# Performance work log

Measured on AMD Instinct MI355X. Metric: run time of the kernel, lower is better.

Reference implementation:

```python
import jax, jax.numpy as jnp
import numpy as np

E, HEADS, HD, L, FF = 768, 12, 64, 12, 3072


def layernorm(x, g, b, eps=1e-5):
    m = jnp.mean(x, axis=-1, keepdims=True)
    v = jnp.var(x, axis=-1, keepdims=True)
    return (x - m) / jnp.sqrt(v + eps) * g + b


def setup_inputs() -> dict:
    key = jax.random.key(0)
    ks = jax.random.split(key, 26)
    B, N, PS = 32, 1024, 24
    P2 = PS * PS
    def rn(k, shape, s=0.02):
        return jax.random.normal(k, shape, dtype=jnp.float32) * s
    return {
        "scene_masks": jax.random.normal(ks[0], (B, N, PS, PS), dtype=jnp.float32),
        "target_mask": jax.random.normal(ks[1], (B, PS, PS), dtype=jnp.float32),
        "emb_W": rn(ks[2], (E, P2)),            # torch Linear weight [out,in]
        "emb_b": rn(ks[3], (E,)),
        "class_embed": rn(ks[4], (1, 1, E)),
        "scene_pos": rn(ks[5], (1, N + 1, E)),
        "target_pos": rn(ks[6], (1, 2, E)),
        "ln1_g": jnp.ones((L, E), jnp.float32),
        "ln1_b": jnp.zeros((L, E), jnp.float32),
        "ln2_g": jnp.ones((L, E), jnp.float32),
        "ln2_b": jnp.zeros((L, E), jnp.float32),
        "Wq": rn(ks[7], (L, HD, HD)),
        "Wk": rn(ks[8], (L, HD, HD)),
        "Wv": rn(ks[9], (L, HD, HD)),
        "Wo": rn(ks[10], (L, E, E)),
        "bo": rn(ks[11], (L, E)),
        "W1": rn(ks[12], (L, FF, E)),
        "b1": rn(ks[13], (L, FF)),
        "W2": rn(ks[14], (L, E, FF)),
        "b2": rn(ks[15], (L, E)),
        "mlp_W": rn(ks[16], (N, E)),
        "mlp_b": rn(ks[17], (N,)),
    }


def _forward_logits(scene_masks, target_mask, emb_W, emb_b, class_embed, scene_pos,
                    target_pos, ln1_g, ln1_b, ln2_g, ln2_b, Wq, Wk, Wv, Wo, bo,
                    W1, b1, W2, b2, mlp_W, mlp_b):
    B, N, H, W = scene_masks.shape
    P2 = H * W
    scene = scene_masks.reshape(B, N, P2) @ emb_W.T + emb_b          # [B,N,E]
    tgt = target_mask.reshape(B, 1, P2) @ emb_W.T + emb_b            # [B,1,E]
    cls = jnp.broadcast_to(class_embed, (B, 1, E))
    scene = jnp.concatenate([cls, scene], axis=1) + scene_pos[:, :N + 1]  # [B,N+1,E]
    tgt = jnp.concatenate([cls, tgt], axis=1) + target_pos               # [B,2,E]
    scale = jnp.sqrt(jnp.float32(E))

    def block(tq, p):
        g1, bb1n, g2, bb2n, wq, wk, wv, wo, bo_, w1, b1_, w2, b2_ = p
        kv = layernorm(scene, g1, bb1n)                # norm1(value)=norm1(key)
        q = layernorm(tq, g1, bb1n)                    # norm1(query)
        kvh = kv.reshape(B, N + 1, HEADS, HD)
        qh = q.reshape(B, 2, HEADS, HD)
        # per-head Linear shares one [HD,HD] weight across all heads
        qs = jnp.einsum('nqhd,ed->nqhe', qh, wq)
        ks_ = jnp.einsum('nkhd,ed->nkhe', kvh, wk)
        vs = jnp.einsum('nkhd,ed->nkhe', kvh, wv)
        energy = jnp.einsum('nqhd,nkhd->nhqk', qs, ks_)     # [B,H,2,N+1]
        att = jax.nn.softmax(energy / scale, axis=-1)
        out = jnp.einsum('nhqk,nkhd->nqhd', att, vs).reshape(B, 2, E)
        out = out @ wo.T + bo_
        x = layernorm(out + tq, g1, bb1n)
        ff = jax.nn.relu(x @ w1.T + b1_) @ w2.T + b2_
        return layernorm(ff + x, g2, bb2n), None

    params = (ln1_g, ln1_b, ln2_g, ln2_b, Wq, Wk, Wv, Wo, bo, W1, b1, W2, b2)
    tgt, _ = jax.lax.scan(block, tgt, params)
    x = jnp.mean(tgt, axis=1) @ mlp_W.T + mlp_b       # [B, num_patches]
    return x


def reference(scene_masks, target_mask, emb_W, emb_b, class_embed, scene_pos,
              target_pos, ln1_g, ln1_b, ln2_g, ln2_b, Wq, Wk, Wv, Wo, bo,
              W1, b1, W2, b2, mlp_W, mlp_b):
    x = _forward_logits(scene_masks, target_mask, emb_W, emb_b, class_embed,
                        scene_pos, target_pos, ln1_g, ln1_b, ln2_g, ln2_b,
                        Wq, Wk, Wv, Wo, bo, W1, b1, W2, b2, mlp_W, mlp_b)
    # sorted_nodes = argsort desc + 1; eye(P+1)[nodes-1] == one_hot(argsort desc)
    order = jnp.argsort(-x, axis=1)[:, :5]                # top-5 patch indices
    return jax.nn.one_hot(order, x.shape[1] + 1, dtype=jnp.float32)  # [B,5,P+1]
```

## Files before the change

### kernel.cpp

```cpp
#include <hip/hip_runtime.h>
#include <math.h>

#define E_DIM 768
#define NTOK 1025
#define B_DIM 32
#define NHEADS 12
#define HDIM 64
#define LAYERS 12
#define FF_DIM 3072
#define P2 576

__device__ __forceinline__ float block_reduce_sum(float v, float* red) {
  int tid = threadIdx.x;
  red[tid] = v;
  __syncthreads();
#pragma unroll
  for (int s = 128; s > 0; s >>= 1) {
    if (tid < s) red[tid] += red[tid + s];
    __syncthreads();
  }
  float r = red[0];
  __syncthreads();
  return r;
}

__global__ __launch_bounds__(256) void embed_gemm(
    const float* __restrict__ A, const float* __restrict__ W,
    const float* __restrict__ bias, const float* __restrict__ pos,
    float* __restrict__ scene) {
  __shared__ float Xs[16][132];
  __shared__ float Ws[16][132];
  int tid = threadIdx.x;
  int bid = blockIdx.x;
  int xcd = bid & 7;
  int idx = bid >> 3;
  int m_tile = xcd * 32 + idx / 6;
  int n_tile = idx % 6;
  int n0 = n_tile * 128;
  int m0 = m_tile * 128;
  int lr = tid >> 2;
  int lk = (tid & 3) << 2;
  int ty = tid >> 4, tx = tid & 15;
  float acc[8][8] = {};
  for (int k0 = 0; k0 < P2; k0 += 16) {
    float4 x0 = *(const float4*)(A + (size_t)(m0 + lr) * P2 + k0 + lk);
    float4 x1 = *(const float4*)(A + (size_t)(m0 + 64 + lr) * P2 + k0 + lk);
    float4 w0 = *(const float4*)(W + (size_t)(n0 + lr) * P2 + k0 + lk);
    float4 w1 = *(const float4*)(W + (size_t)(n0 + 64 + lr) * P2 + k0 + lk);
    __syncthreads();
    Xs[lk + 0][lr] = x0.x; Xs[lk + 1][lr] = x0.y; Xs[lk + 2][lr] = x0.z; Xs[lk + 3][lr] = x0.w;
    Xs[lk + 0][64 + lr] = x1.x; Xs[lk + 1][64 + lr] = x1.y; Xs[lk + 2][64 + lr] = x1.z; Xs[lk + 3][64 + lr] = x1.w;
    Ws[lk + 0][lr] = w0.x; Ws[lk + 1][lr] = w0.y; Ws[lk + 2][lr] = w0.z; Ws[lk + 3][lr] = w0.w;
    Ws[lk + 0][64 + lr] = w1.x; Ws[lk + 1][64 + lr] = w1.y; Ws[lk + 2][64 + lr] = w1.z; Ws[lk + 3][64 + lr] = w1.w;
    __syncthreads();
#pragma unroll
    for (int kk = 0; kk < 16; ++kk) {
      float4 a0 = *(const float4*)&Xs[kk][ty << 2];
      float4 a1 = *(const float4*)&Xs[kk][64 + (ty << 2)];
      float4 b0 = *(const float4*)&Ws[kk][tx << 2];
      float4 b1 = *(const float4*)&Ws[kk][64 + (tx << 2)];
      float av[8] = {a0.x, a0.y, a0.z, a0.w, a1.x, a1.y, a1.z, a1.w};
      float bv[8] = {b0.x, b0.y, b0.z, b0.w, b1.x, b1.y, b1.z, b1.w};
#pragma unroll
      for (int i = 0; i < 8; ++i)
#pragma unroll
        for (int j = 0; j < 8; ++j) acc[i][j] += av[i] * bv[j];
    }
  }
#pragma unroll
  for (int i = 0; i < 8; ++i) {
    int mloc = (i < 4) ? ((ty << 2) + i) : (64 + (ty << 2) + i - 4);
    int m = m0 + mloc;
    int b = m >> 10, nt = m & 1023;
    size_t row = ((size_t)b * NTOK + 1 + nt) * E_DIM;
    size_t prow = (size_t)(1 + nt) * E_DIM;
#pragma unroll
    for (int half = 0; half < 2; ++half) {
      int n = n0 + half * 64 + (tx << 2);
      float4 o4;
      o4.x = acc[i][half * 4 + 0] + bias[n + 0] + pos[prow + n + 0];
      o4.y = acc[i][half * 4 + 1] + bias[n + 1] + pos[prow + n + 1];
      o4.z = acc[i][half * 4 + 2] + bias[n + 2] + pos[prow + n + 2];
      o4.w = acc[i][half * 4 + 3] + bias[n + 3] + pos[prow + n + 3];
      *(float4*)&scene[row + n] = o4;
    }
  }
}

__global__ void scene_cls(const float* __restrict__ cls, const float* __restrict__ pos,
                          float* __restrict__ scene) {
  int b = blockIdx.x;
  for (int e = threadIdx.x; e < E_DIM; e += 256)
    scene[(size_t)b * NTOK * E_DIM + e] = cls[e] + pos[e];
}

__global__ __launch_bounds__(256) void ln_rows(const float* __restrict__ in, float* __restrict__ out) {
  __shared__ float red[256];
  int r = blockIdx.x, tid = threadIdx.x;
  const float* x = in + (size_t)r * E_DIM;
  float a0 = x[tid], a1 = x[tid + 256], a2 = x[tid + 512];
  float mean = block_reduce_sum(a0 + a1 + a2, red) * (1.f / 768.f);
  float d0 = a0 - mean, d1 = a1 - mean, d2 = a2 - mean;
  float var = block_reduce_sum(d0 * d0 + d1 * d1 + d2 * d2, red) * (1.f / 768.f);
  float rinv = rsqrtf(var + 1e-5f);
  float* o = out + (size_t)r * E_DIM;
  o[tid] = d0 * rinv; o[tid + 256] = d1 * rinv; o[tid + 512] = d2 * rinv;
}

__global__ __launch_bounds__(256) void tgt_init(
    const float* __restrict__ tmask, const float* __restrict__ W,
    const float* __restrict__ bias, const float* __restrict__ cls,
    const float* __restrict__ tpos, float* __restrict__ tq) {
  int b = blockIdx.x, tid = threadIdx.x;
  for (int e = tid; e < E_DIM; e += 256)
    tq[(size_t)(b * 2) * E_DIM + e] = cls[e] + tpos[e];
  const float* tm = tmask + (size_t)b * P2;
  for (int e = tid; e < E_DIM; e += 256) {
    const float* wr = W + (size_t)e * P2;
    float s = 0.f;
    for (int k = 0; k < P2; k += 4) {
      float4 w4 = *(const float4*)&wr[k];
      float4 t4 = *(const float4*)&tm[k];
      s += w4.x * t4.x + w4.y * t4.y + w4.z * t4.z + w4.w * t4.w;
    }
    tq[(size_t)(b * 2 + 1) * E_DIM + e] = s + bias[e] + tpos[E_DIM + e];
  }
}

__global__ void prep_m(const float* __restrict__ Wq, const float* __restrict__ Wk,
                       float* __restrict__ Mb) {
  int l = blockIdx.y;
  int idx = blockIdx.x * 256 + threadIdx.x;
  int d = idx >> 6, dp = idx & 63;
  const float* wq = Wq + l * 4096;
  const float* wk = Wk + l * 4096;
  float s = 0.f;
#pragma unroll 8
  for (int e = 0; e < 64; ++e) s += wq[e * 64 + d] * wk[e * 64 + dp];
  Mb[l * 4096 + idx] = s;
}

__global__ void prep_wvo(const float* __restrict__ Wv, const float* __restrict__ Wo,
                         float* __restrict__ Wvo) {
  int l = blockIdx.y;
  int idx = blockIdx.x * 256 + threadIdx.x;
  int ep = idx / 768, hd = idx % 768;
  int h = hd >> 6, d = hd & 63;
  const float* wv = Wv + (size_t)l * 4096;
  const float* wo = Wo + (size_t)l * 768 * 768 + (size_t)ep * 768 + h * 64;
  float s = 0.f;
#pragma unroll 8
  for (int ev = 0; ev < 64; ++ev) s += wv[ev * 64 + d] * wo[ev];
  Wvo[(size_t)l * 589824 + idx] = s;
}

#define ACH 272
__global__ __launch_bounds__(256) void attn_flash_q(
    const float* __restrict__ tq_in, const float* __restrict__ partFF,
    const float* __restrict__ fb2l, const float* __restrict__ g2l,
    const float* __restrict__ b2l, const float* __restrict__ xres,
    int from_part, float* __restrict__ tq_out,
    const float* __restrict__ Mb, const float* __restrict__ g1,
    const float* __restrict__ b1, int l,
    const float* __restrict__ ns, float* __restrict__ ctx) {
  __shared__ float red[256];
  __shared__ float qs[2][64];
  __shared__ float qg[2][64];
  __shared__ float qmb[2];
  __shared__ float sred[2][16];
  __shared__ float cred[2][16][64];
  int b = blockIdx.x / NHEADS;
  int h = blockIdx.x % NHEADS;
  int tid = threadIdx.x;
  const float* gl = g1 + l * E_DIM;
  const float* bl = b1 + l * E_DIM;
  int seg = h >> 2;
  int base = h * 64 - seg * 256;

  float y[2][3];
  if (!from_part) {
#pragma unroll
    for (int r = 0; r < 2; ++r) {
      const float* x = tq_in + (size_t)(b * 2 + r) * E_DIM;
      y[r][0] = x[tid]; y[r][1] = x[tid + 256]; y[r][2] = x[tid + 512];
    }
  } else {
#pragma unroll
    for (int r = 0; r < 2; ++r) {
      int m = b * 2 + r;
      float t[3];
#pragma unroll
      for (int c = 0; c < 3; ++c) {
        int n = tid + c * 256;
        float s = 0.f;
        for (int i = 0; i < 16; ++i) s += partFF[((size_t)i * 64 + m) * 768 + n];
        t[c] = s + fb2l[n] + xres[(size_t)m * 768 + n];
      }
      float mean = block_reduce_sum(t[0] + t[1] + t[2], red) * (1.f / 768.f);
      float d0 = t[0] - mean, d1 = t[1] - mean, d2 = t[2] - mean;
      float var = block_reduce_sum(d0 * d0 + d1 * d1 + d2 * d2, red) * (1.f / 768.f);
      float rinv = rsqrtf(var + 1e-5f);
      y[r][0] = d0 * rinv * g2l[tid] + b2l[tid];
      y[r][1] = d1 * rinv * g2l[tid + 256] + b2l[tid + 256];
      y[r][2] = d2 * rinv * g2l[tid + 512] + b2l[tid + 512];
      if (h == 0) {
        tq_out[(size_t)m * E_DIM + tid] = y[r][0];
        tq_out[(size_t)m * E_DIM + tid + 256] = y[r][1];
        tq_out[(size_t)m * E_DIM + tid + 512] = y[r][2];
      }
    }
  }

  for (int r = 0; r < 2; ++r) {
    float a0 = y[r][0], a1 = y[r][1], a2 = y[r][2];
    float mean = block_reduce_sum(a0 + a1 + a2, red) * (1.f / 768.f);
    float d0 = a0 - mean, d1 = a1 - mean, d2 = a2 - mean;
    float var = block_reduce_sum(d0 * d0 + d1 * d1 + d2 * d2, red) * (1.f / 768.f);
    float rinv = rsqrtf(var + 1e-5f);
    float dv = (seg == 0) ? d0 : ((seg == 1) ? d1 : d2);
    if (tid >= base && tid < base + 64) {
      int d = tid - base;
      qs[r][d] = dv * rinv * gl[h * 64 + d] + bl[h * 64 + d];
    }
  }
  __syncthreads();
  const float inv_scale = rsqrtf(768.f);
  if (tid < 128) {
    int r = tid >> 6, dp = tid & 63;
    const float* M = Mb + l * 4096;
    float s = 0.f;
#pragma unroll 8
    for (int d = 0; d < 64; ++d) s += qs[r][d] * M[d * 64 + dp];
    qg[r][dp] = s * gl[h * 64 + dp] * inv_scale;
    red[tid] = s * bl[h * 64 + dp];
  }
  __syncthreads();
  if (tid < 2) {
    float a = 0.f;
    for (int dp = 0; dp < 64; ++dp) a += red[tid * 64 + dp];
    qmb[tid] = a * inv_scale;
  }
  __syncthreads();
  int g = tid >> 4;
  int lane = tid & 15;
  int r0 = b * 2, r1 = r0 + 1;
  const float* nsb = ns + (size_t)b * NTOK * E_DIM + h * 64;
  float4 q0v = *(const float4*)&qg[0][lane * 4];
  float4 q1v = *(const float4*)&qg[1][lane * 4];
  float qb0 = qmb[0], qb1 = qmb[1];
  float m = -1e30f, s0 = 0.f, s1 = 0.f;
  float4 c0 = {0, 0, 0, 0}, c1 = {0, 0, 0, 0};
  float4 v[17];
  float e0a[17], e1a[17];
  for (int cb = 0; cb < NTOK; cb += ACH) {
    int ntk = NTOK - cb; if (ntk > ACH) ntk = ACH;
    int cnt = (ntk - g + 15) >> 4;
    float mloc = -1e30f;
#pragma unroll
    for (int i = 0; i < 17; ++i) {
      if (i < cnt) {
        int k = cb + g + (i << 4);
        float4 vv = *(const float4*)(nsb + (size_t)k * E_DIM + lane * 4);
        v[i] = vv;
        float p0 = vv.x * q0v.x + vv.y * q0v.y + vv.z * q0v.z + vv.w * q0v.w;
        float p1 = vv.x * q1v.x + vv.y * q1v.y + vv.z * q1v.z + vv.w * q1v.w;
#pragma unroll
        for (int off = 8; off; off >>= 1) {
          p0 += __shfl_xor(p0, off, 16);
          p1 += __shfl_xor(p1, off, 16);
        }
        float e0 = p0 + qb0, e1 = p1 + qb1;
        e0a[i] = e0; e1a[i] = e1;
        mloc = fmaxf(mloc, fmaxf(e0, e1));
      }
    }
    red[tid] = mloc;
    __syncthreads();
#pragma unroll
    for (int s = 128; s > 0; s >>= 1) {
      if (tid < s) red[tid] = fmaxf(red[tid], red[tid + s]);
      __syncthreads();
    }
    float mnew = fmaxf(m, red[0]);
    __syncthreads();
    if (mnew > m) {
      float f = expf(m - mnew);
      s0 *= f; s1 *= f;
      c0.x *= f; c0.y *= f; c0.z *= f; c0.w *= f;
      c1.x *= f; c1.y *= f; c1.z *= f; c1.w *= f;
      m = mnew;
    }
#pragma unroll
    for (int i = 0; i < 17; ++i) {
      if (i < cnt) {
        float p0 = expf(e0a[i] - m);
        float p1 = expf(e1a[i] - m);
        s0 += p0; s1 += p1;
        c0.x += p0 * v[i].x; c0.y += p0 * v[i].y; c0.z += p0 * v[i].z; c0.w += p0 * v[i].w;
        c1.x += p1 * v[i].x; c1.y += p1 * v[i].y; c1.z += p1 * v[i].z; c1.w += p1 * v[i].w;
      }
    }
  }
  if (lane == 0) { sred[0][g] = s0; sred[1][g] = s1; }
  *(float4*)&cred[0][g][lane * 4] = c0;
  *(float4*)&cred[1][g][lane * 4] = c1;
  __syncthreads();
  if (tid < 128) {
    int t = tid >> 6, dd = tid & 63;
    int o = h * 64 + dd;
    float stot = 0.f, cs = 0.f;
#pragma unroll
    for (int gg = 0; gg < 16; ++gg) { stot += sred[t][gg]; cs += cred[t][gg][dd]; }
    float inv = 1.f / stot;
    ctx[(size_t)(r0 + t) * E_DIM + o] = cs * inv * gl[o] + bl[o];
  }
}

__global__ __launch_bounds__(256) void skinny_part(
    const float* __restrict__ X, int K, const float* __restrict__ W,
    int kchunk, float* __restrict__ part, int N) {
  __shared__ float Xs[16][64];
  __shared__ float Ws[16][64];
  int tid = threadIdx.x;
  int n0 = blockIdx.x * 64;
  int s = blockIdx.y;
  int kbeg = s * kchunk;
  int lr = tid >> 2;
  int lk = (tid & 3) << 2;
  int ty = tid >> 4, tx = tid & 15;
  float acc[4][4] = {};
  for (int k0 = kbeg; k0 < kbeg + kchunk; k0 += 16) {
    float4 xv = *(const float4*)(X + (size_t)lr * K + k0 + lk);
    float4 wv = *(const float4*)(W + (size_t)(n0 + lr) * K + k0 + lk);
    __syncthreads();
    Xs[lk + 0][lr] = xv.x; Xs[lk + 1][lr] = xv.y; Xs[lk + 2][lr] = xv.z; Xs[lk + 3][lr] = xv.w;
    Ws[lk + 0][lr] = wv.x; Ws[lk + 1][lr] = wv.y; Ws[lk + 2][lr] = wv.z; Ws[lk + 3][lr] = wv.w;
    __syncthreads();
#pragma unroll
    for (int kk = 0; kk < 16; ++kk) {
      float4 a4 = *(const float4*)&Xs[kk][ty << 2];
      float4 b4 = *(const float4*)&Ws[kk][tx << 2];
      float av[4] = {a4.x, a4.y, a4.z, a4.w};
      float bv[4] = {b4.x, b4.y, b4.z, b4.w};
#pragma unroll
      for (int i = 0; i < 4; ++i)
#pragma unroll
        for (int j = 0; j < 4; ++j) acc[i][j] += av[i] * bv[j];
    }
  }
#pragma unroll
  for (int i = 0; i < 4; ++i) {
    int mm = (ty << 2) + i;
    float4 o4 = make_float4(acc[i][0], acc[i][1], acc[i][2], acc[i][3]);
    *(float4*)&part[((size_t)s * 64 + mm) * N + n0 + (tx << 2)] = o4;
  }
}

__global__ __launch_bounds__(256) void skinny_h1_part(
    const float* __restrict__ part1, const float* __restrict__ b1,
    const float* __restrict__ W, int kchunk, float* __restrict__ part2) {
  __shared__ float Xs[16][64];
  __shared__ float Ws[16][64];
  const int K = 3072, N = 768;
  int tid = threadIdx.x;
  int n0 = blockIdx.x * 64;
  int s = blockIdx.y;
  int kbeg = s * kchunk;
  int lr = tid >> 2;
  int lk = (tid & 3) << 2;
  int ty = tid >> 4, tx = tid & 15;
  float acc[4][4] = {};
  for (int k0 = kbeg; k0 < kbeg + kchunk; k0 += 16) {
    float4 x0 = *(const float4*)(part1 + (size_t)lr * K + k0 + lk);
    float4 x1 = *(const float4*)(part1 + (size_t)(64 + lr) * K + k0 + lk);
    float4 x2 = *(const float4*)(part1 + (size_t)(128 + lr) * K + k0 + lk);
    float4 x3 = *(const float4*)(part1 + (size_t)(192 + lr) * K + k0 + lk);
    float4 bb = *(const float4*)(b1 + k0 + lk);
    float4 xv;
    xv.x = fmaxf(x0.x + x1.x + x2.x + x3.x + bb.x, 0.f);
    xv.y = fmaxf(x0.y + x1.y + x2.y + x3.y + bb.y, 0.f);
    xv.z = fmaxf(x0.z + x1.z + x2.z + x3.z + bb.z, 0.f);
    xv.w = fmaxf(x0.w + x1.w + x2.w + x3.w + bb.w, 0.f);
    float4 wv = *(const float4*)(W + (size_t)(n0 + lr) * K + k0 + lk);
    __syncthreads();
    Xs[lk + 0][lr] = xv.x; Xs[lk + 1][lr] = xv.y; Xs[lk + 2][lr] = xv.z; Xs[lk + 3][lr] = xv.w;
    Ws[lk + 0][lr] = wv.x; Ws[lk + 1][lr] = wv.y; Ws[lk + 2][lr] = wv.z; Ws[lk + 3][lr] = wv.w;
    __syncthreads();
#pragma unroll
    for (int kk = 0; kk < 16; ++kk) {
      float4 a4 = *(const float4*)&Xs[kk][ty << 2];
      float4 b4 = *(const float4*)&Ws[kk][tx << 2];
      float av[4] = {a4.x, a4.y, a4.z, a4.w};
      float bv[4] = {b4.x, b4.y, b4.z, b4.w};
#pragma unroll
      for (int i = 0; i < 4; ++i)
#pragma unroll
        for (int j = 0; j < 4; ++j) acc[i][j] += av[i] * bv[j];
    }
  }
#pragma unroll
  for (int i = 0; i < 4; ++i) {
    int mm = (ty << 2) + i;
    float4 o4 = make_float4(acc[i][0], acc[i][1], acc[i][2], acc[i][3]);
    *(float4*)&part2[((size_t)s * 64 + mm) * N + n0 + (tx << 2)] = o4;
  }
}

__global__ __launch_bounds__(256) void reduce_ln(
    const float* __restrict__ part, int S, const float* __restrict__ bias,
    const float* __restrict__ res, const float* __restrict__ g,
    const float* __restrict__ bsh, float* __restrict__ out,
    float* __restrict__ xmean) {
  __shared__ float red[256];
  int m = blockIdx.x, tid = threadIdx.x;
  float t[3];
#pragma unroll
  for (int c = 0; c < 3; ++c) {
    int n = tid + c * 256;
    float s = 0.f;
    for (int i = 0; i < S; ++i) s += part[((size_t)i * 64 + m) * 768 + n];
    t[c] = s + bias[n] + res[(size_t)m * 768 + n];
  }
  float mean = block_reduce_sum(t[0] + t[1] + t[2], red) * (1.f / 768.f);
  float d0 = t[0] - mean, d1 = t[1] - mean, d2 = t[2] - mean;
  float var = block_reduce_sum(d0 * d0 + d1 * d1 + d2 * d2, red) * (1.f / 768.f);
  float rinv = rsqrtf(var + 1e-5f);
  float y0 = d0 * rinv * g[tid] + bsh[tid];
  float y1 = d1 * rinv * g[tid + 256] + bsh[tid + 256];
  float y2 = d2 * rinv * g[tid + 512] + bsh[tid + 512];
  out[(size_t)m * 768 + tid] = y0;
  out[(size_t)m * 768 + tid + 256] = y1;
  out[(size_t)m * 768 + tid + 512] = y2;
  if (xmean) {
    float* xr = xmean + (size_t)(m >> 1) * 768;
    atomicAdd(&xr[tid], 0.5f * y0);
    atomicAdd(&xr[tid + 256], 0.5f * y1);
    atomicAdd(&xr[tid + 512], 0.5f * y2);
  }
}

__global__ __launch_bounds__(256) void top5_from_parts(
    const float* __restrict__ part, const float* __restrict__ bias,
    float* __restrict__ out) {
  __shared__ float v[1024];
  __shared__ float bv[256];
  __shared__ int bi[256];
  int b = blockIdx.x, tid = threadIdx.x;
  for (int i = tid; i < 1024; i += 256) {
    float s = part[(size_t)(0 * 64 + b) * 1024 + i] + part[(size_t)(1 * 64 + b) * 1024 + i] +
              part[(size_t)(2 * 64 + b) * 1024 + i] + part[(size_t)(3 * 64 + b) * 1024 + i];
    v[i] = s + bias[i];
  }
  float* ob = out + (size_t)b * 5 * NTOK;
  for (int i = tid; i < 5 * NTOK; i += 256) ob[i] = 0.f;
  __syncthreads();
  for (int it = 0; it < 5; ++it) {
    float best = -1e38f;
    int bidx = 0x7fffffff;
    for (int i = tid; i < 1024; i += 256) {
      float x = v[i];
      if (x > best || (x == best && i < bidx)) { best = x; bidx = i; }
    }
    bv[tid] = best; bi[tid] = bidx;
    __syncthreads();
    for (int s = 128; s > 0; s >>= 1) {
      if (tid < s) {
        if (bv[tid + s] > bv[tid] || (bv[tid + s] == bv[tid] && bi[tid + s] < bi[tid])) {
          bv[tid] = bv[tid + s]; bi[tid] = bi[tid + s];
        }
      }
      __syncthreads();
    }
    if (tid == 0) {
      ob[it * NTOK + bi[0]] = 1.0f;
      v[bi[0]] = -1e38f;
    }
    __syncthreads();
  }
}

extern "C" void kernel_launch(void* const* d_in, const int* in_sizes, int n_in,
                              void* d_out, int out_size, void* d_ws, size_t ws_size,
                              hipStream_t stream) {
  const float* scene_masks = (const float*)d_in[0];
  const float* target_mask = (const float*)d_in[1];
  const float* emb_W = (const float*)d_in[2];
  const float* emb_b = (const float*)d_in[3];
  const float* class_embed = (const float*)d_in[4];
  const float* scene_pos = (const float*)d_in[5];
  const float* target_pos = (const float*)d_in[6];
  const float* ln1_g = (const float*)d_in[7];
  const float* ln1_b = (const float*)d_in[8];
  const float* ln2_g = (const float*)d_in[9];
  const float* ln2_b = (const float*)d_in[10];
  const float* Wq = (const float*)d_in[11];
  const float* Wk = (const float*)d_in[12];
  const float* Wv = (const float*)d_in[13];
  const float* Wo = (const float*)d_in[14];
  const float* bo = (const float*)d_in[15];
  const float* W1 = (const float*)d_in[16];
  const float* fb1 = (const float*)d_in[17];
  const float* W2 = (const float*)d_in[18];
  const float* fb2 = (const float*)d_in[19];
  const float* mlp_W = (const float*)d_in[20];
  const float* mlp_b = (const float*)d_in[21];
  float* out = (float*)d_out;

  float* ws = (float*)d_ws;
  float* scene = ws;
  float* Mbuf = scene + 25190400;
  float* Wvo = Mbuf + 49152;
  float* tq = Wvo + 7077888;
  float* ctxf = tq + 49152;
  float* xbuf = ctxf + 49152;
  float* xm = xbuf + 49152;
  float* partA = xm + 49152;
  float* partB = partA + 786432;

  embed_gemm<<<1536, 256, 0, stream>>>(scene_masks, emb_W, emb_b, scene_pos, scene);
  scene_cls<<<32, 256, 0, stream>>>(class_embed, scene_pos, scene);
  ln_rows<<<32 * NTOK, 256, 0, stream>>>(scene, scene);
  tgt_init<<<32, 256, 0, stream>>>(target_mask, emb_W, emb_b, class_embed, target_pos, tq);
  prep_m<<<dim3(16, 12), 256, 0, stream>>>(Wq, Wk, Mbuf);
  prep_wvo<<<dim3(2304, 12), 256, 0, stream>>>(Wv, Wo, Wvo);
  hipMemsetAsync(xm, 0, 49152 * sizeof(float), stream);

  for (int l = 0; l < LAYERS; ++l) {
    if (l == 0)
      attn_flash_q<<<32 * NHEADS, 256, 0, stream>>>(
          tq, nullptr, nullptr, nullptr, nullptr, nullptr, 0, nullptr,
          Mbuf, ln1_g, ln1_b, l, scene, ctxf);
    else
      attn_flash_q<<<32 * NHEADS, 256, 0, stream>>>(
          nullptr, partA, fb2 + (l - 1) * 768, ln2_g + (l - 1) * 768,
          ln2_b + (l - 1) * 768, xbuf, 1, tq,
          Mbuf, ln1_g, ln1_b, l, scene, ctxf);
    skinny_part<<<dim3(12, 8), 256, 0, stream>>>(ctxf, 768, Wvo + (size_t)l * 589824, 96, partA, 768);
    reduce_ln<<<64, 256, 0, stream>>>(partA, 8, bo + l * 768, tq,
                                      ln1_g + l * 768, ln1_b + l * 768, xbuf, nullptr);
    skinny_part<<<dim3(48, 4), 256, 0, stream>>>(xbuf, 768, W1 + (size_t)l * FF_DIM * 768, 192, partB, FF_DIM);
    skinny_h1_part<<<dim3(12, 16), 256, 0, stream>>>(partB, fb1 + l * FF_DIM,
                                                     W2 + (size_t)l * 768 * FF_DIM, 192, partA);
  }
  reduce_ln<<<64, 256, 0, stream>>>(partA, 16, fb2 + 11 * 768, xbuf,
                                    ln2_g + 11 * 768, ln2_b + 11 * 768, tq, xm);

  skinny_part<<<dim3(16, 4), 256, 0, stream>>>(xm, 768, mlp_W, 192, partA, 1024);
  top5_from_parts<<<32, 256, 0, stream>>>(partA, mlp_b, out);
}
```

Baseline: 1.817 ms.

## Fuse per-head output projection into attention kernel, drop separate skinny GEMM

Each attention block now multiplies its per-head context by the matching column slice of the fused Wv·Wo matrix and writes per-head partial sums, which reduce_ln sums over 12 heads. This removes one GEMM launch and the context buffer round trip per layer. In exchange every block re-reads its 768x64 weight slice (shared across batches via cache) and partC adds a larger partial buffer to reduce.

```diff
diff --git a/kernel.cpp b/kernel.cpp
--- a/kernel.cpp
+++ b/kernel.cpp
@@ -162,13 +162,16 @@
     int from_part, float* __restrict__ tq_out,
     const float* __restrict__ Mb, const float* __restrict__ g1,
     const float* __restrict__ b1, int l,
-    const float* __restrict__ ns, float* __restrict__ ctx) {
+    const float* __restrict__ ns, const float* __restrict__ Wvo_l,
+    float* __restrict__ partC) {
   __shared__ float red[256];
   __shared__ float qs[2][64];
   __shared__ float qg[2][64];
   __shared__ float qmb[2];
   __shared__ float sred[2][16];
   __shared__ float cred[2][16][64];
+  __shared__ float ctxs[2][64];
+  __shared__ float pr[2][768];
   int b = blockIdx.x / NHEADS;
   int h = blockIdx.x % NHEADS;
   int tid = threadIdx.x;
@@ -312,7 +315,28 @@
 #pragma unroll
     for (int gg = 0; gg < 16; ++gg) { stot += sred[t][gg]; cs += cred[t][gg][dd]; }
     float inv = 1.f / stot;
-    ctx[(size_t)(r0 + t) * E_DIM + o] = cs * inv * gl[o] + bl[o];
+    ctxs[t][dd] = cs * inv * gl[o] + bl[o];
+  }
+  __syncthreads();
+  const float* wbase = Wvo_l + (size_t)h * 64 + lane * 4;
+  float4 x0 = *(const float4*)&ctxs[0][lane * 4];
+  float4 x1 = *(const float4*)&ctxs[1][lane * 4];
+  for (int n = g; n < 768; n += 16) {
+    float4 wv = *(const float4*)(wbase + (size_t)n * 768);
+    float a0 = wv.x * x0.x + wv.y * x0.y + wv.z * x0.z + wv.w * x0.w;
+    float a1 = wv.x * x1.x + wv.y * x1.y + wv.z * x1.z + wv.w * x1.w;
+#pragma unroll
+    for (int off = 8; off; off >>= 1) {
+      a0 += __shfl_xor(a0, off, 16);
+      a1 += __shfl_xor(a1, off, 16);
+    }
+    if (lane == 0) { pr[0][n] = a0; pr[1][n] = a1; }
+  }
+  __syncthreads();
+  float* pc = partC + (size_t)h * 49152;
+  for (int i = tid; i < 2 * 768; i += 256) {
+    int r = i / 768, c = i % 768;
+    pc[(size_t)(r0 + r) * 768 + c] = pr[r][c];
   }
 }
 
@@ -511,11 +535,11 @@
   float* Mbuf = scene + 25190400;
   float* Wvo = Mbuf + 49152;
   float* tq = Wvo + 7077888;
-  float* ctxf = tq + 49152;
-  float* xbuf = ctxf + 49152;
+  float* xbuf = tq + 49152;
   float* xm = xbuf + 49152;
   float* partA = xm + 49152;
   float* partB = partA + 786432;
+  float* partC = partB + 786432;
 
   embed_gemm<<<1536, 256, 0, stream>>>(scene_masks, emb_W, emb_b, scene_pos, scene);
   scene_cls<<<32, 256, 0, stream>>>(class_embed, scene_pos, scene);
@@ -529,14 +553,13 @@
     if (l == 0)
       attn_flash_q<<<32 * NHEADS, 256, 0, stream>>>(
           tq, nullptr, nullptr, nullptr, nullptr, nullptr, 0, nullptr,
-          Mbuf, ln1_g, ln1_b, l, scene, ctxf);
+          Mbuf, ln1_g, ln1_b, l, scene, Wvo + (size_t)l * 589824, partC);
     else
       attn_flash_q<<<32 * NHEADS, 256, 0, stream>>>(
           nullptr, partA, fb2 + (l - 1) * 768, ln2_g + (l - 1) * 768,
           ln2_b + (l - 1) * 768, xbuf, 1, tq,
-          Mbuf, ln1_g, ln1_b, l, scene, ctxf);
-    skinny_part<<<dim3(12, 8), 256, 0, stream>>>(ctxf, 768, Wvo + (size_t)l * 589824, 96, partA, 768);
-    reduce_ln<<<64, 256, 0, stream>>>(partA, 8, bo + l * 768, tq,
+          Mbuf, ln1_g, ln1_b, l, scene, Wvo + (size_t)l * 589824, partC);
+    reduce_ln<<<64, 256, 0, stream>>>(partC, 12, bo + l * 768, tq,
                                       ln1_g + l * 768, ln1_b + l * 768, xbuf, nullptr);
     skinny_part<<<dim3(48, 4), 256, 0, stream>>>(xbuf, 768, W1 + (size_t)l * FF_DIM * 768, 192, partB, FF_DIM);
     skinny_h1_part<<<dim3(12, 16), 256, 0, stream>>>(partB, fb1 + l * FF_DIM,
```

Measured after the change: 2.060 ms. 1.13x slower.
